# Performance work log

Hardware: AMD Instinct MI355X
Metric: run time of the kernel (lower is better)

The kernel has to match this reference:

```python
import jax, jax.numpy as jnp
import numpy as np

B, S, D = 2, 400, 512  # batch, seq (src == tgt for self-attention), dim; attn_hidden=0 so d == D


def setup_inputs() -> dict:
    key = jax.random.key(0)
    ks = jax.random.split(key, 9)
    inv = 1.0 / np.sqrt(D)
    return {
        "input": jax.random.normal(ks[0], (B, S, D), jnp.float32),
        "memory_bank": jax.random.normal(ks[1], (B, S, D), jnp.float32),
        # lengths in [S//2, S], guaranteed >= 2 so no row is fully masked
        "memory_lengths": jax.random.randint(ks[2], (B,), S // 2, S + 1, jnp.int32),
        "Wq": jax.random.normal(ks[3], (D, D), jnp.float32) * inv,   # linear_query.weight^T
        "bq": jax.random.normal(ks[4], (D,), jnp.float32) * inv,      # linear_query.bias
        "Wc": jax.random.normal(ks[5], (D, D), jnp.float32) * inv,   # linear_context.weight^T
        "v": jax.random.normal(ks[6], (D,), jnp.float32) * inv,       # v.weight (d -> 1)
        "Wout": jax.random.normal(ks[7], (2 * D, D), jnp.float32) * inv,  # linear_out.weight^T
        "bout": jax.random.normal(ks[8], (D,), jnp.float32) * inv,
    }


def reference(input, memory_bank, memory_lengths, Wq, bq, Wc, v, Wout, bout):
    b, s, d = memory_bank.shape
    # Bahdanau/mlp score: v^T tanh(Wq q + b + Wc h)
    wq = jnp.einsum("btd,de->bte", input, Wq) + bq            # [B,T,d]
    uh = jnp.einsum("bsd,de->bse", memory_bank, Wc)           # [B,S,d]
    wquh = jnp.tanh(wq[:, :, None, :] + uh[:, None, :, :])    # [B,T,S,d] big intermediate
    scores = jnp.einsum("btse,e->bts", wquh, v)               # [B,T,S]
    # padding mask (j < length) with self position masked out on the diagonal
    pos = jnp.arange(s)
    key_mask = pos[None, :] < memory_lengths[:, None]         # [B,S]
    mask = key_mask[:, None, :] & (pos[:, None] != pos[None, :])  # [B,T,S]
    scores = jnp.where(mask, scores, -jnp.inf)
    align = jax.nn.softmax(scores, axis=2)                    # [B,T,S]
    c = jnp.einsum("bts,bsd->btd", align, memory_bank)        # context [B,T,D]
    concat_c = jnp.concatenate([c, input], axis=2)            # [B,T,2D]
    attn_h = jnp.einsum("btf,fd->btd", concat_c, Wout) + bout # [B,T,D]
    # mlp variant: no sigmoid gating
    return attn_h.transpose(1, 0, 2), align.transpose(1, 0, 2)  # [T,B,D], [T,B,S]
```

## Files before the change

kernel.cpp:

```cpp
#include <hip/hip_runtime.h>
#include <math.h>

#define BB 2
#define SS 400
#define DD 512
#define TWO_LOG2E 2.8853900817779268f

#if __has_builtin(__builtin_amdgcn_exp2f)
#define EXP2F(x) __builtin_amdgcn_exp2f(x)
#else
#define EXP2F(x) exp2f(x)
#endif
#define RCPF(x) __builtin_amdgcn_rcpf(x)

#define EAOFF 0
#define MOFF 409600
#define EB4OFF 819200
#define XOFF 1228800

typedef __bf16 bf16x8 __attribute__((ext_vector_type(8)));
typedef float floatx16 __attribute__((ext_vector_type(16)));

__global__ __launch_bounds__(256) void k0_all(
    const float* __restrict__ Wq, const float* __restrict__ Wc,
    const float* __restrict__ Wout, const float* __restrict__ input,
    const float* __restrict__ mbk, unsigned short* __restrict__ wt,
    unsigned short* __restrict__ ahi, unsigned short* __restrict__ alo)
{
    const int gid = blockIdx.x;
    if (gid < 1024) {
        const int g   = gid >> 9;
        const int rem = gid & 511;
        const int k0  = (rem & 15) * 32;
        const int n0  = (rem >> 4) * 32;

        __shared__ float tile[32][33];
        const int nn  = threadIdx.x & 31;
        const int kk0 = threadIdx.x >> 5;
        const int n   = n0 + nn;

        #pragma unroll
        for (int p = 0; p < 4; ++p) {
            const int k = k0 + kk0 + p * 8;
            float val;
            if (n0 < 512) val = (g ? Wc : Wq)[(size_t)k * 512 + n];
            else          val = Wout[((size_t)(g ? k : 512 + k)) * 512 + (n - 512)];
            tile[kk0 + p * 8][nn] = val;
        }
        __syncthreads();

        const int kc = threadIdx.x & 31;
        #pragma unroll
        for (int p = 0; p < 4; ++p) {
            const int nl = (threadIdx.x >> 5) + p * 8;
            const __bf16 h = (__bf16)tile[kc][nl];
            wt[((size_t)(g * 1024 + n0 + nl)) * 512 + k0 + kc] =
                __builtin_bit_cast(unsigned short, h);
        }
    } else {
        const int cid = gid - 1024;
        const int g   = (cid >= 400) ? 1 : 0;
        const int i4  = (cid - g * 400) * 256 + threadIdx.x;
        const float4 a = ((const float4*)(g ? mbk : input))[i4];
        ushort4 h, l;
        #pragma unroll
        for (int j = 0; j < 4; ++j) {
            const float av = (&a.x)[j];
            const __bf16 hh = (__bf16)av;
            (&h.x)[j] = __builtin_bit_cast(unsigned short, hh);
            const __bf16 ll = (__bf16)(av - (float)hh);
            (&l.x)[j] = __builtin_bit_cast(unsigned short, ll);
        }
        ((ushort4*)(ahi + (size_t)g * 409600))[i4] = h;
        ((ushort4*)(alo + (size_t)g * 409600))[i4] = l;
    }
}

__global__ __launch_bounds__(64) void k1_mfma(
    const unsigned short* __restrict__ ahi, const unsigned short* __restrict__ alo,
    const unsigned short* __restrict__ wt, const float* __restrict__ bq,
    const float* __restrict__ bout, float* __restrict__ ws,
    float* __restrict__ out0)
{
    const int lane = threadIdx.x;
    const int mt   = blockIdx.x;
    const int np   = blockIdx.y;
    const int g    = blockIdx.z;
    const int m    = lane & 31;
    const int kh   = lane >> 5;
    const int n0   = np * 64;

    const size_t arow = ((size_t)g * 800 + mt * 32 + m) * 512 + kh * 8;
    const unsigned short* __restrict__ ah = ahi + arow;
    const unsigned short* __restrict__ al = alo + arow;
    const unsigned short* __restrict__ w0 =
        wt + ((size_t)(g * 1024 + n0 + m)) * 512 + kh * 8;
    const unsigned short* __restrict__ w1 = w0 + (size_t)32 * 512;

    floatx16 acc0h, acc0l, acc1h, acc1l;
    #pragma unroll
    for (int i = 0; i < 16; ++i) { acc0h[i] = 0.f; acc0l[i] = 0.f;
                                   acc1h[i] = 0.f; acc1l[i] = 0.f; }

    #pragma unroll 4
    for (int ks = 0; ks < 32; ++ks) {
        const bf16x8 va0 = *(const bf16x8*)(ah + ks * 16);
        const bf16x8 va1 = *(const bf16x8*)(al + ks * 16);
        const bf16x8 bh0 = *(const bf16x8*)(w0 + ks * 16);
        const bf16x8 bh1 = *(const bf16x8*)(w1 + ks * 16);

        acc0h = __builtin_amdgcn_mfma_f32_32x32x16_bf16(va0, bh0, acc0h, 0, 0, 0);
        acc0l = __builtin_amdgcn_mfma_f32_32x32x16_bf16(va1, bh0, acc0l, 0, 0, 0);
        acc1h = __builtin_amdgcn_mfma_f32_32x32x16_bf16(va0, bh1, acc1h, 0, 0, 0);
        acc1l = __builtin_amdgcn_mfma_f32_32x32x16_bf16(va1, bh1, acc1l, 0, 0, 0);
    }

    const floatx16 c0 = acc0h + acc0l;
    const floatx16 c1 = acc1h + acc1l;
    const int rbase = kh * 4;

    #pragma unroll
    for (int r = 0; r < 16; ++r) {
        const int row  = (r & 3) + 8 * (r >> 2) + rbase;
        const int grow = mt * 32 + row;
        const int bi   = (grow >= SS) ? 1 : 0;
        const int rl   = grow - bi * SS;
        #pragma unroll
        for (int u = 0; u < 2; ++u) {
            const float val  = u ? c1[r] : c0[r];
            const int   gcol = n0 + u * 32 + m;
            if (g == 0) {
                if (gcol < 512) {
                    ws[EAOFF + (size_t)grow * 512 + gcol] =
                        EXP2F(TWO_LOG2E * (val + bq[gcol]));
                } else {
                    const int d = gcol - 512;
                    out0[((size_t)(rl * BB + bi)) * 512 + d] = val + bout[d];
                }
            } else {
                if (gcol < 512) {
                    ws[EB4OFF + (size_t)((bi * 128 + (gcol >> 2)) * SS + rl) * 4
                       + (gcol & 3)] = EXP2F(TWO_LOG2E * val);
                } else {
                    ws[MOFF + (size_t)grow * 512 + (gcol - 512)] = val;
                }
            }
        }
    }
}

__global__ __launch_bounds__(512) void k2_attn(
    const float* __restrict__ ws, const float* __restrict__ v,
    const int* __restrict__ lens, float* __restrict__ out1,
    float* __restrict__ out0)
{
    const int tp = blockIdx.x;
    const int b  = blockIdx.y;
    const int t0 = tp * 2;
    const int t1 = t0 + 1;
    const int tid = threadIdx.x;
    const int s   = tid;
    const int sidx = (s < SS) ? s : 0;
    const int len  = lens[b];

    __shared__ float lea[2][512];
    __shared__ float lv[512];
    __shared__ float lal[SS][2];
    __shared__ float wred0[8], wred1[8];

    lv[tid] = v[tid];
    lea[0][tid] = ws[EAOFF + (size_t)(b * SS + t0) * 512 + tid];
    lea[1][tid] = ws[EAOFF + (size_t)(b * SS + t1) * 512 + tid];
    __syncthreads();

    const float4* __restrict__ eb4 =
        (const float4*)(ws + EB4OFF) + (size_t)b * 128 * SS + sidx;

    float acc0 = 0.f, acc1 = 0.f;
    #pragma unroll 4
    for (int e4 = 0; e4 < 128; ++e4) {
        const float4 eb  = eb4[(size_t)e4 * SS];
        const float4 vv  = *(const float4*)&lv[e4 * 4];
        const float4 ea0 = *(const float4*)&lea[0][e4 * 4];
        const float4 ea1 = *(const float4*)&lea[1][e4 * 4];
        #pragma unroll
        for (int j = 0; j < 4; ++j) {
            const float ebv = (&eb.x)[j];
            const float vj  = (&vv.x)[j];
            acc0 = fmaf(vj, RCPF(fmaf((&ea0.x)[j], ebv, 1.f)), acc0);
            acc1 = fmaf(vj, RCPF(fmaf((&ea1.x)[j], ebv, 1.f)), acc1);
        }
    }

    const bool v0 = (s < SS) && (s < len) && (s != t0);
    const bool v1 = (s < SS) && (s < len) && (s != t1);
    const float sc0 = v0 ? -2.f * acc0 : -INFINITY;
    const float sc1 = v1 ? -2.f * acc1 : -INFINITY;

    const int wid  = tid >> 6;
    const int lane = tid & 63;

    float m0 = sc0, m1 = sc1;
    #pragma unroll
    for (int off = 32; off > 0; off >>= 1) {
        m0 = fmaxf(m0, __shfl_xor(m0, off));
        m1 = fmaxf(m1, __shfl_xor(m1, off));
    }
    if (lane == 0) { wred0[wid] = m0; wred1[wid] = m1; }
    __syncthreads();
    float mx0 = wred0[0], mx1 = wred1[0];
    #pragma unroll
    for (int w = 1; w < 8; ++w) {
        mx0 = fmaxf(mx0, wred0[w]);
        mx1 = fmaxf(mx1, wred1[w]);
    }
    __syncthreads();

    const float p0 = v0 ? __expf(sc0 - mx0) : 0.f;
    const float p1 = v1 ? __expf(sc1 - mx1) : 0.f;
    float s0v = p0, s1v = p1;
    #pragma unroll
    for (int off = 32; off > 0; off >>= 1) {
        s0v += __shfl_xor(s0v, off);
        s1v += __shfl_xor(s1v, off);
    }
    if (lane == 0) { wred0[wid] = s0v; wred1[wid] = s1v; }
    __syncthreads();
    float tot0 = wred0[0], tot1 = wred1[0];
    #pragma unroll
    for (int w = 1; w < 8; ++w) { tot0 += wred0[w]; tot1 += wred1[w]; }
    const float inv0 = RCPF(tot0);
    const float inv1 = RCPF(tot1);

    if (s < SS) {
        const float a0 = p0 * inv0;
        const float a1 = p1 * inv1;
        out1[((size_t)(t0 * BB) + b) * SS + s] = a0;
        out1[((size_t)(t1 * BB) + b) * SS + s] = a1;
        lal[s][0] = a0;
        lal[s][1] = a1;
    }
    __syncthreads();

    const float* __restrict__ Mb = ws + MOFF + (size_t)b * SS * DD;
    const int d = tid;
    float c0a = 0.f, c0b = 0.f, c1a = 0.f, c1b = 0.f;
    #pragma unroll 4
    for (int sp = 0; sp < SS; sp += 2) {
        const float mv0 = Mb[(size_t)sp * DD + d];
        const float mv1 = Mb[(size_t)(sp + 1) * DD + d];
        const float2 a0 = *(const float2*)&lal[sp][0];
        const float2 a1 = *(const float2*)&lal[sp + 1][0];
        c0a = fmaf(a0.x, mv0, c0a);
        c1a = fmaf(a0.y, mv0, c1a);
        c0b = fmaf(a1.x, mv1, c0b);
        c1b = fmaf(a1.y, mv1, c1b);
    }
    const size_t o0 = ((size_t)(t0 * BB) + b) * DD + d;
    const size_t o1 = ((size_t)(t1 * BB) + b) * DD + d;
    out0[o0] += c0a + c0b;
    out0[o1] += c1a + c1b;
}

extern "C" void kernel_launch(void* const* d_in, const int* in_sizes, int n_in,
                              void* d_out, int out_size, void* d_ws, size_t ws_size,
                              hipStream_t stream)
{
    const float* input = (const float*)d_in[0];
    const float* mbk   = (const float*)d_in[1];
    const int*   lens  = (const int*)d_in[2];
    const float* Wq    = (const float*)d_in[3];
    const float* bq    = (const float*)d_in[4];
    const float* Wc    = (const float*)d_in[5];
    const float* v     = (const float*)d_in[6];
    const float* Wout  = (const float*)d_in[7];
    const float* bout  = (const float*)d_in[8];

    float* out0 = (float*)d_out;
    float* out1 = out0 + (size_t)BB * SS * DD;
    float* ws   = (float*)d_ws;
    unsigned short* x16 = (unsigned short*)(ws + XOFF);
    unsigned short* wt  = x16;
    unsigned short* ahi = x16 + 1048576;
    unsigned short* alo = ahi + 819200;

    hipLaunchKernelGGL(k0_all, dim3(1824), dim3(256), 0, stream,
                       Wq, Wc, Wout, input, mbk, wt, ahi, alo);
    hipLaunchKernelGGL(k1_mfma, dim3(25, 16, 2), dim3(64), 0, stream,
                       ahi, alo, wt, bq, bout, ws, out0);
    hipLaunchKernelGGL(k2_attn, dim3(200, 2), dim3(512), 0, stream,
                       ws, v, lens, out1, out0);
}
```

Measured before the change: 146.1 us.

## Pair reciprocals in score loop and skip idle wavefront in attention kernel

The score loop now combines two tanh-style terms per reciprocal by computing (v0*d1+v1*d0)/(d0*d1), halving the number of RCP instructions. The eighth wavefront (threads 448-511, all beyond S) now skips the score computation, and the reduction uses 7 partial slots. Separate shared buffers for max and sum let one barrier be dropped. The risk is overflow or precision loss in the product d0*d1 when the exponentials are large.

```diff
diff --git a/kernel.cpp b/kernel.cpp
--- a/kernel.cpp
+++ b/kernel.cpp
@@ -154,10 +154,10 @@
     const int* __restrict__ lens, float* __restrict__ out1,
     float* __restrict__ out0)
 {
-    const int tp = blockIdx.x;
-    const int b  = blockIdx.y;
-    const int t0 = tp * 2;
-    const int t1 = t0 + 1;
+    const int tp  = blockIdx.x;
+    const int b   = blockIdx.y;
+    const int t0  = tp * 2;
+    const int t1  = t0 + 1;
     const int tid = threadIdx.x;
     const int s   = tid;
     const int sidx = (s < SS) ? s : 0;
@@ -166,100 +166,112 @@
     __shared__ float lea[2][512];
     __shared__ float lv[512];
     __shared__ float lal[SS][2];
-    __shared__ float wred0[8], wred1[8];
+    __shared__ float wredm0[7], wredm1[7], wreds0[7], wreds1[7];
 
     lv[tid] = v[tid];
     lea[0][tid] = ws[EAOFF + (size_t)(b * SS + t0) * 512 + tid];
     lea[1][tid] = ws[EAOFF + (size_t)(b * SS + t1) * 512 + tid];
     __syncthreads();
 
-    const float4* __restrict__ eb4 =
-        (const float4*)(ws + EB4OFF) + (size_t)b * 128 * SS + sidx;
-
-    float acc0 = 0.f, acc1 = 0.f;
-    #pragma unroll 4
-    for (int e4 = 0; e4 < 128; ++e4) {
-        const float4 eb  = eb4[(size_t)e4 * SS];
-        const float4 vv  = *(const float4*)&lv[e4 * 4];
-        const float4 ea0 = *(const float4*)&lea[0][e4 * 4];
-        const float4 ea1 = *(const float4*)&lea[1][e4 * 4];
-        #pragma unroll
-        for (int j = 0; j < 4; ++j) {
-            const float ebv = (&eb.x)[j];
-            const float vj  = (&vv.x)[j];
-            acc0 = fmaf(vj, RCPF(fmaf((&ea0.x)[j], ebv, 1.f)), acc0);
-            acc1 = fmaf(vj, RCPF(fmaf((&ea1.x)[j], ebv, 1.f)), acc1);
-        }
-    }
-
-    const bool v0 = (s < SS) && (s < len) && (s != t0);
-    const bool v1 = (s < SS) && (s < len) && (s != t1);
-    const float sc0 = v0 ? -2.f * acc0 : -INFINITY;
-    const float sc1 = v1 ? -2.f * acc1 : -INFINITY;
-
     const int wid  = tid >> 6;
     const int lane = tid & 63;
-
-    float m0 = sc0, m1 = sc1;
+    const bool active = (tid < 448);
+
+    float sc0 = -INFINITY, sc1 = -INFINITY;
+    bool v0 = false, v1 = false;
+
+    if (active) {
+        const float4* __restrict__ eb4 =
+            (const float4*)(ws + EB4OFF) + (size_t)b * 128 * SS + sidx;
+
+        float a00 = 0.f, a01 = 0.f, a10 = 0.f, a11 = 0.f;
+        #pragma unroll 8
+        for (int e4 = 0; e4 < 128; ++e4) {
+            const float4 eb = eb4[(size_t)e4 * SS];
+            const float4 vv = *(const float4*)&lv[e4 * 4];
+            const float4 e0 = *(const float4*)&lea[0][e4 * 4];
+            const float4 e1 = *(const float4*)&lea[1][e4 * 4];
+            float d0, d1;
+            d0 = fmaf(e0.x, eb.x, 1.f); d1 = fmaf(e0.y, eb.y, 1.f);
+            a00 = fmaf(fmaf(vv.x, d1, vv.y * d0), RCPF(d0 * d1), a00);
+            d0 = fmaf(e0.z, eb.z, 1.f); d1 = fmaf(e0.w, eb.w, 1.f);
+            a01 = fmaf(fmaf(vv.z, d1, vv.w * d0), RCPF(d0 * d1), a01);
+            d0 = fmaf(e1.x, eb.x, 1.f); d1 = fmaf(e1.y, eb.y, 1.f);
+            a10 = fmaf(fmaf(vv.x, d1, vv.y * d0), RCPF(d0 * d1), a10);
+            d0 = fmaf(e1.z, eb.z, 1.f); d1 = fmaf(e1.w, eb.w, 1.f);
+            a11 = fmaf(fmaf(vv.z, d1, vv.w * d0), RCPF(d0 * d1), a11);
+        }
+        const float acc0 = (a00 + a01);
+        const float acc1 = (a10 + a11);
+
+        v0 = (s < SS) && (s < len) && (s != t0);
+        v1 = (s < SS) && (s < len) && (s != t1);
+        sc0 = v0 ? -2.f * acc0 : -INFINITY;
+        sc1 = v1 ? -2.f * acc1 : -INFINITY;
+
+        float m0 = sc0, m1 = sc1;
+        #pragma unroll
+        for (int off = 32; off > 0; off >>= 1) {
+            m0 = fmaxf(m0, __shfl_xor(m0, off));
+            m1 = fmaxf(m1, __shfl_xor(m1, off));
+        }
+        if (lane == 0) { wredm0[wid] = m0; wredm1[wid] = m1; }
+    }
+    __syncthreads();
+
+    float mx0 = wredm0[0], mx1 = wredm1[0];
     #pragma unroll
-    for (int off = 32; off > 0; off >>= 1) {
-        m0 = fmaxf(m0, __shfl_xor(m0, off));
-        m1 = fmaxf(m1, __shfl_xor(m1, off));
-    }
-    if (lane == 0) { wred0[wid] = m0; wred1[wid] = m1; }
+    for (int w = 1; w < 7; ++w) {
+        mx0 = fmaxf(mx0, wredm0[w]);
+        mx1 = fmaxf(mx1, wredm1[w]);
+    }
+
+    float p0 = 0.f, p1 = 0.f;
+    if (active) {
+        p0 = v0 ? __expf(sc0 - mx0) : 0.f;
+        p1 = v1 ? __expf(sc1 - mx1) : 0.f;
+        float s0v = p0, s1v = p1;
+        #pragma unroll
+        for (int off = 32; off > 0; off >>= 1) {
+            s0v += __shfl_xor(s0v, off);
+            s1v += __shfl_xor(s1v, off);
+        }
+        if (lane == 0) { wreds0[wid] = s0v; wreds1[wid] = s1v; }
+    }
     __syncthreads();
-    float mx0 = wred0[0], mx1 = wred1[0];
+
+    float tot0 = wreds0[0], tot1 = wreds1[0];
     #pragma unroll
-    for (int w = 1; w < 8; ++w) {
-        mx0 = fmaxf(mx0, wred0[w]);
-        mx1 = fmaxf(mx1, wred1[w]);
-    }
-    __syncthreads();
-
-    const float p0 = v0 ? __expf(sc0 - mx0) : 0.f;
-    const float p1 = v1 ? __expf(sc1 - mx1) : 0.f;
-    float s0v = p0, s1v = p1;
-    #pragma unroll
-    for (int off = 32; off > 0; off >>= 1) {
-        s0v += __shfl_xor(s0v, off);
-        s1v += __shfl_xor(s1v, off);
-    }
-    if (lane == 0) { wred0[wid] = s0v; wred1[wid] = s1v; }
-    __syncthreads();
-    float tot0 = wred0[0], tot1 = wred1[0];
-    #pragma unroll
-    for (int w = 1; w < 8; ++w) { tot0 += wred0[w]; tot1 += wred1[w]; }
+    for (int w = 1; w < 7; ++w) { tot0 += wreds0[w]; tot1 += wreds1[w]; }
     const float inv0 = RCPF(tot0);
     const float inv1 = RCPF(tot1);
 
-    if (s < SS) {
-        const float a0 = p0 * inv0;
-        const float a1 = p1 * inv1;
-        out1[((size_t)(t0 * BB) + b) * SS + s] = a0;
-        out1[((size_t)(t1 * BB) + b) * SS + s] = a1;
-        lal[s][0] = a0;
-        lal[s][1] = a1;
+    if (active && s < SS) {
+        const float al0 = p0 * inv0;
+        const float al1 = p1 * inv1;
+        out1[((size_t)(t0 * BB) + b) * SS + s] = al0;
+        out1[((size_t)(t1 * BB) + b) * SS + s] = al1;
+        lal[s][0] = al0;
+        lal[s][1] = al1;
     }
     __syncthreads();
 
     const float* __restrict__ Mb = ws + MOFF + (size_t)b * SS * DD;
     const int d = tid;
-    float c0a = 0.f, c0b = 0.f, c1a = 0.f, c1b = 0.f;
+    float c0 = 0.f, c1 = 0.f, c2 = 0.f, c3 = 0.f;
     #pragma unroll 4
     for (int sp = 0; sp < SS; sp += 2) {
         const float mv0 = Mb[(size_t)sp * DD + d];
         const float mv1 = Mb[(size_t)(sp + 1) * DD + d];
-        const float2 a0 = *(const float2*)&lal[sp][0];
-        const float2 a1 = *(const float2*)&lal[sp + 1][0];
-        c0a = fmaf(a0.x, mv0, c0a);
-        c1a = fmaf(a0.y, mv0, c1a);
-        c0b = fmaf(a1.x, mv1, c0b);
-        c1b = fmaf(a1.y, mv1, c1b);
-    }
-    const size_t o0 = ((size_t)(t0 * BB) + b) * DD + d;
-    const size_t o1 = ((size_t)(t1 * BB) + b) * DD + d;
-    out0[o0] += c0a + c0b;
-    out0[o1] += c1a + c1b;
+        const float2 l0 = *(const float2*)&lal[sp][0];
+        const float2 l1 = *(const float2*)&lal[sp + 1][0];
+        c0 = fmaf(l0.x, mv0, c0);
+        c1 = fmaf(l0.y, mv0, c1);
+        c2 = fmaf(l1.x, mv1, c2);
+        c3 = fmaf(l1.y, mv1, c3);
+    }
+    out0[((size_t)(t0 * BB) + b) * DD + d] += c0 + c2;
+    out0[((size_t)(t1 * BB) + b) * DD + d] += c1 + c3;
 }
 
 extern "C" void kernel_launch(void* const* d_in, const int* in_sizes, int n_in,
```

Result: slower. 166.3 us (+13.8%).
